# Kernel optimization log

Measured on AMD Instinct MI355X. Metric: run time of the kernel, lower is better.

Reference implementation:

```python
import jax, jax.numpy as jnp
import numpy as np

B, S, HID = 2, 2048, 2048
H, KVH, D = 16, 2, 256
ROT = 64  # head_dim * partial_rotary_factor (0.25)
EPS = 1e-6


def setup_inputs() -> dict:
    key = jax.random.key(0)
    ks = jax.random.split(key, 6)
    hidden_states = jax.random.normal(ks[0], (B, S, HID), dtype=jnp.float32)
    # real partial-RoPE cos/sin, rope_theta = 1e6
    inv_freq = 1.0 / (1e6 ** (np.arange(0, ROT, 2, dtype=np.float32) / ROT))
    pos = np.arange(S, dtype=np.float32)
    freqs = np.outer(pos, inv_freq)                      # [S, ROT/2]
    emb = np.concatenate([freqs, freqs], axis=-1)        # [S, ROT]
    cos = jnp.broadcast_to(jnp.asarray(np.cos(emb)), (B, S, ROT))
    sin = jnp.broadcast_to(jnp.asarray(np.sin(emb)), (B, S, ROT))
    sc = 0.02
    Wq = jax.random.normal(ks[1], (HID, H * D * 2), dtype=jnp.float32) * sc
    Wk = jax.random.normal(ks[2], (HID, KVH * D), dtype=jnp.float32) * sc
    Wv = jax.random.normal(ks[3], (HID, KVH * D), dtype=jnp.float32) * sc
    Wo = jax.random.normal(ks[4], (H * D, HID), dtype=jnp.float32) * sc
    q_norm_w = jnp.zeros((D,), dtype=jnp.float32)
    k_norm_w = jnp.zeros((D,), dtype=jnp.float32)
    return dict(hidden_states=hidden_states, cos=cos, sin=sin, Wq=Wq, Wk=Wk,
                Wv=Wv, Wo=Wo, q_norm_w=q_norm_w, k_norm_w=k_norm_w)


def _rms_norm(x, w):
    x32 = x.astype(jnp.float32)
    out = x32 * jax.lax.rsqrt(jnp.mean(x32 * x32, axis=-1, keepdims=True) + EPS)
    return (out * (1.0 + w.astype(jnp.float32))).astype(x.dtype)


def _rotate_half(x):
    x1, x2 = jnp.split(x, 2, axis=-1)
    return jnp.concatenate([-x2, x1], axis=-1)


def _apply_rope(x, cos, sin):
    # x: [B,S,N,D]; cos/sin: [B,S,ROT] -> unsqueeze head dim
    c = cos[:, :, None, :]
    s = sin[:, :, None, :]
    x_rot, x_pass = x[..., :ROT], x[..., ROT:]
    x_rot = x_rot * c + _rotate_half(x_rot) * s
    return jnp.concatenate([x_rot, x_pass], axis=-1)


def reference(hidden_states, cos, sin, Wq, Wk, Wv, Wo, q_norm_w, k_norm_w):
    b, s, _ = hidden_states.shape
    # gated Q projection: view as (b,s,H,2D), chunk last dim into query + gate
    qg = (hidden_states @ Wq).reshape(b, s, H, 2 * D)
    q, gate = qg[..., :D], qg[..., D:]
    gate = gate.reshape(b, s, H * D)
    k = (hidden_states @ Wk).reshape(b, s, KVH, D)
    v = (hidden_states @ Wv).reshape(b, s, KVH, D)
    # per-head RMSNorm then partial RoPE
    q = _apply_rope(_rms_norm(q, q_norm_w), cos, sin)
    k = _apply_rope(_rms_norm(k, k_norm_w), cos, sin)
    # GQA: repeat kv heads
    rep = H // KVH
    k = jnp.repeat(k, rep, axis=2)  # [b,s,H,D]
    v = jnp.repeat(v, rep, axis=2)
    # causal SDPA (bsnd layout)
    scale = 1.0 / jnp.sqrt(jnp.asarray(D, dtype=q.dtype))
    scores = jnp.einsum('bqhd,bkhd->bhqk', q, k) * scale
    causal = jnp.tril(jnp.ones((s, s), dtype=bool))
    scores = jnp.where(causal[None, None], scores, jnp.finfo(scores.dtype).min)
    probs = jax.nn.softmax(scores, axis=-1)
    attn = jnp.einsum('bhqk,bkhd->bqhd', probs, v).reshape(b, s, H * D)
    # output gating + projection
    attn = attn * jax.nn.sigmoid(gate)
    return attn @ Wo
```

## Files before the change

kernel.cpp:

```cpp
#include <hip/hip_runtime.h>
#include <cstdint>
#include <cstddef>

#define S_   2048
#define H_   16
#define KVH_ 2
#define D_   256

typedef __attribute__((ext_vector_type(4))) float          float4v;
typedef __attribute__((ext_vector_type(4))) float          floatx4;
typedef __attribute__((ext_vector_type(8))) unsigned short ushort8v;
typedef __attribute__((ext_vector_type(4))) unsigned short ushort4v;
typedef __attribute__((ext_vector_type(8))) short          short8;

__device__ __forceinline__ float bf2f(unsigned short u){
  union{float f; unsigned int i;} v; v.i = ((unsigned int)u)<<16; return v.f;
}
__device__ __forceinline__ unsigned short f2bf(float f){
  union{float f; unsigned int i;} v; v.f = f;
  unsigned int r = v.i + 0x7FFFu + ((v.i>>16)&1u);
  return (unsigned short)(r>>16);
}
__device__ __forceinline__ void gld16(const void* g, void* l){
  __builtin_amdgcn_global_load_lds(
      (const __attribute__((address_space(1))) unsigned int*)g,
      (__attribute__((address_space(3))) unsigned int*)l, 16, 0, 0);
}

__global__ __launch_bounds__(256) void conv_k(
    const float* __restrict__ in, unsigned short* __restrict__ out)
{
  const size_t i = ((size_t)blockIdx.x*256 + threadIdx.x)*8;
  float4v a0 = *(const float4v*)(in + i), a1 = *(const float4v*)(in + i + 4);
  ushort8v u;
#pragma unroll
  for (int e=0;e<4;e++){ u[e]=f2bf(a0[e]); u[e+4]=f2bf(a1[e]); }
  *(ushort8v*)(out + i) = u;
}

__global__ __launch_bounds__(256) void tconv_k(
    const float* __restrict__ in, unsigned short* __restrict__ out, int K, int N)
{
  __shared__ unsigned short T[64][72];
  const int n0 = blockIdx.x<<6, k0 = blockIdx.y<<6;
  const int t = threadIdx.x, r = t>>2, c = (t&3)<<4;
  const float* ip = in + (size_t)(k0+r)*N + n0 + c;
  float4v a0=*(const float4v*)ip,     a1=*(const float4v*)(ip+4);
  float4v a2=*(const float4v*)(ip+8), a3=*(const float4v*)(ip+12);
  ushort8v u0,u1;
#pragma unroll
  for (int e=0;e<4;e++){ u0[e]=f2bf(a0[e]); u0[e+4]=f2bf(a1[e]);
                         u1[e]=f2bf(a2[e]); u1[e+4]=f2bf(a3[e]); }
  *(ushort8v*)&T[r][c] = u0; *(ushort8v*)&T[r][c+8] = u1;
  __syncthreads();
  ushort8v o0,o1;
#pragma unroll
  for (int j=0;j<8;j++){ o0[j]=T[c+j][r]; o1[j]=T[c+8+j][r]; }
  unsigned short* op = out + (size_t)(n0+r)*K + k0 + c;
  *(ushort8v*)op = o0; *(ushort8v*)(op+8) = o1;
}

template<int MODE>
__global__ __launch_bounds__(256,2) void gemm_k(
    const unsigned short* __restrict__ A, const unsigned short* __restrict__ Bt,
    void* __restrict__ out0, void* __restrict__ out1, int K, int N)
{
  __shared__ unsigned short Ash[2][128*32];
  __shared__ unsigned short Bsh[2][128*32];
  const int tid  = threadIdx.x;
  const int gm   = blockIdx.x<<7, gn = blockIdx.y<<7;
  const int lane = tid & 63, wave = tid >> 6;
  const int quad = lane >> 4, col = lane & 15;
  const int wm   = (wave>>1)<<6, wn = (wave&1)<<6;
  const int rowoff = lane>>2;
  const int chunk  = (lane&3) ^ (rowoff&3);
  const int ra0 = wave<<4, ra1 = 64 + (wave<<4);
  const unsigned short* Ab = A  + (size_t)gm*K;
  const unsigned short* Bb = Bt + (size_t)gn*K;
  const int cf = (quad ^ (col&3))<<3;

  floatx4 acc[4][4];
#pragma unroll
  for (int i=0;i<4;i++)
#pragma unroll
    for (int j=0;j<4;j++) acc[i][j] = (floatx4)0.f;

  const int niter = K>>5;
  {
    const int ko = chunk*8;
    gld16(Ab + (size_t)(ra0+rowoff)*K + ko, &Ash[0][ra0*32]);
    gld16(Ab + (size_t)(ra1+rowoff)*K + ko, &Ash[0][ra1*32]);
    gld16(Bb + (size_t)(ra0+rowoff)*K + ko, &Bsh[0][ra0*32]);
    gld16(Bb + (size_t)(ra1+rowoff)*K + ko, &Bsh[0][ra1*32]);
  }
  for (int it=0; it<niter; ++it){
    const int buf = it&1;
    __syncthreads();
    if (it+1 < niter){
      const int ko = (it+1)*32 + chunk*8;
      gld16(Ab + (size_t)(ra0+rowoff)*K + ko, &Ash[buf^1][ra0*32]);
      gld16(Ab + (size_t)(ra1+rowoff)*K + ko, &Ash[buf^1][ra1*32]);
      gld16(Bb + (size_t)(ra0+rowoff)*K + ko, &Bsh[buf^1][ra0*32]);
      gld16(Bb + (size_t)(ra1+rowoff)*K + ko, &Bsh[buf^1][ra1*32]);
    }
    short8 af[4], bfr[4];
#pragma unroll
    for (int mi=0;mi<4;mi++) af[mi]  = *(const short8*)&Ash[buf][(wm+mi*16+col)*32 + cf];
#pragma unroll
    for (int ni=0;ni<4;ni++) bfr[ni] = *(const short8*)&Bsh[buf][(wn+ni*16+col)*32 + cf];
#pragma unroll
    for (int mi=0;mi<4;mi++)
#pragma unroll
      for (int ni=0;ni<4;ni++)
        acc[mi][ni] = __builtin_amdgcn_mfma_f32_16x16x32_bf16(af[mi], bfr[ni], acc[mi][ni], 0,0,0);
  }

#pragma unroll
  for (int mi=0;mi<4;mi++){
#pragma unroll
    for (int r=0;r<4;r++){
      const int m = gm + wm + mi*16 + quad*4 + r;
      const int b = m >> 11, s = m & 2047;
#pragma unroll
      for (int ni=0;ni<4;ni++){
        const int n = gn + wn + ni*16 + col;
        const float v = acc[mi][ni][r];
        if (MODE==0){
          if (n < 8192){
            const int h = n >> 9, dd = n & 511;
            if (dd < 256)
              ((unsigned short*)out0)[(((size_t)b*H_ + h)*S_ + s)*D_ + dd] = f2bf(v);
            else
              ((unsigned short*)out1)[((size_t)m*H_ + h)*D_ + (dd-256)] = f2bf(v);
          } else {
            const int n2 = n - 8192;
            if (n2 < 512){
              const int kvh = n2 >> 8, dd = n2 & 255;
              ((unsigned short*)out0)[(size_t)(67108864/2) + (((size_t)b*KVH_ + kvh)*S_ + s)*D_ + dd] = f2bf(v);
            } else {
              const int nv2 = n2 - 512;
              const int kvh = nv2 >> 8, dd = nv2 & 255;
              ((unsigned short*)out0)[(size_t)(71303168/2) + ((((size_t)b*KVH_ + kvh)*64 + (s>>5))*256 + dd)*32 + (s&31)] = f2bf(v);
            }
          }
        } else {
          ((float*)out0)[(size_t)m*N + n] = v;
        }
      }
    }
  }
}

__global__ __launch_bounds__(256,2) void normrope_k(
    unsigned short* __restrict__ x, const float* __restrict__ w,
    const float* __restrict__ cosp, const float* __restrict__ sinp, int heads)
{
  const int lane = threadIdx.x & 63;
  const int row  = blockIdx.x*4 + (threadIdx.x>>6);
  const int s    = row & (S_-1);
  const int b    = (row / S_) / heads;
  unsigned short* xp = x + (size_t)row * D_;
  const int d = lane*4;
  ushort4v xv = *(const ushort4v*)(xp + d);
  float v0=bf2f(xv[0]), v1=bf2f(xv[1]), v2=bf2f(xv[2]), v3=bf2f(xv[3]);
  float ss = v0*v0+v1*v1+v2*v2+v3*v3;
#pragma unroll
  for (int off=1; off<64; off<<=1) ss += __shfl_xor(ss, off, 64);
  const float rstd = rsqrtf(ss*(1.f/256.f) + 1e-6f);
  float nv[4] = { v0*rstd*(1.f+w[d]),   v1*rstd*(1.f+w[d+1]),
                  v2*rstd*(1.f+w[d+2]), v3*rstd*(1.f+w[d+3]) };
  float ov[4];
#pragma unroll
  for (int j=0;j<4;j++){
    const float other = __shfl_xor(nv[j], 8, 64);
    float o = nv[j];
    if (lane < 16){
      const float c  = cosp[((size_t)b*S_+s)*64 + d + j];
      const float sn = sinp[((size_t)b*S_+s)*64 + d + j];
      o = (lane < 8) ? (nv[j]*c - other*sn) : (nv[j]*c + other*sn);
    }
    ov[j] = o;
  }
  ushort4v ou;
#pragma unroll
  for (int j=0;j<4;j++) ou[j] = f2bf(ov[j]);
  *(ushort4v*)(xp + d) = ou;
}

__global__ __launch_bounds__(256,2) void flash_k(
    const unsigned short* __restrict__ qb, const unsigned short* __restrict__ kbp,
    const unsigned short* __restrict__ vtp, const unsigned short* __restrict__ gb,
    unsigned short* __restrict__ ob)
{
  __shared__ unsigned short SH[2*8192 + 2*8192 + 4*2*640];
  unsigned short* Kb0 = SH;
  unsigned short* Vb0 = SH + 16384;
  const int gid = blockIdx.x;
  const int p   = gid & 7;
  const int h   = (gid>>3) & 15;
  const int b   = gid >> 7;
  const int kvh = h >> 3;
  const int tid = threadIdx.x, wave = tid>>6, lane = tid&63;
  const int quad = lane>>4, col = lane&15;
  unsigned short* Psh = SH + 32768 + wave*1280;

  int kOff[4], vOff[4];
#pragma unroll
  for (int j=0;j<4;j++){
    const int krow = wave*8 + j*2 + (lane>>5);
    kOff[j] = krow*256 + ((lane&31) ^ (krow&7))*8;
    const int vrow = wave*64 + j*16 + (lane>>2);
    vOff[j] = vrow*32 + ((lane&3) ^ (vrow&3))*8;
  }
  const unsigned short* Kg = kbp + ((size_t)b*KVH_ + kvh)*S_*D_;
  const unsigned short* Vg = vtp + ((size_t)b*KVH_ + kvh)*S_*D_;

  for (int sp=0; sp<2; ++sp){
    const int qt = sp ? (15-p) : p;
    const int qw = qt*128 + wave*32;
    const int nch = 4*qt + 4;

    short8 qf[2][8];
#pragma unroll
    for (int m=0;m<2;m++){
      const unsigned short* qr = qb + (((size_t)b*H_ + h)*S_ + (qw + m*16 + col))*D_;
#pragma unroll
      for (int dc=0; dc<8; ++dc) qf[m][dc] = *(const short8*)(qr + dc*32 + quad*8);
    }
    floatx4 O[2][16];
#pragma unroll
    for (int m=0;m<2;m++)
#pragma unroll
      for (int i=0;i<16;i++) O[m][i] = (floatx4)0.f;
    float lacc[2][4] = {{0.f,0.f,0.f,0.f},{0.f,0.f,0.f,0.f}};

    __syncthreads();
#pragma unroll
    for (int j=0;j<4;j++){
      gld16(Kg + kOff[j], Kb0 + wave*2048 + j*512);
      gld16(Vg + vOff[j], Vb0 + wave*2048 + j*512);
    }

    int buf = 0;
    for (int kc=0; kc<nch; ++kc){
      __syncthreads();
      if (kc+1 < nch){
        const unsigned short* kg = Kg + (size_t)(kc+1)*8192;
        const unsigned short* vg = Vg + (size_t)(kc+1)*8192;
        unsigned short* kl = Kb0 + (buf^1)*8192 + wave*2048;
        unsigned short* vl = Vb0 + (buf^1)*8192 + wave*2048;
#pragma unroll
        for (int j=0;j<4;j++){
          gld16(kg + kOff[j], kl + j*512);
          gld16(vg + vOff[j], vl + j*512);
        }
      }
      const unsigned short* Ksh = Kb0 + buf*8192;
      const unsigned short* Vt  = Vb0 + buf*8192;

      floatx4 sc[2][2];
#pragma unroll
      for (int m=0;m<2;m++){ sc[m][0]=(floatx4)0.f; sc[m][1]=(floatx4)0.f; }
#pragma unroll
      for (int dc=0; dc<8; ++dc){
#pragma unroll
        for (int nt=0;nt<2;nt++){
          const int row = nt*16+col;
          short8 kf = *(const short8*)&Ksh[row*256 + (((dc*4+quad) ^ (row&7))<<3)];
          sc[0][nt] = __builtin_amdgcn_mfma_f32_16x16x32_bf16(qf[0][dc], kf, sc[0][nt], 0,0,0);
          sc[1][nt] = __builtin_amdgcn_mfma_f32_16x16x32_bf16(qf[1][dc], kf, sc[1][nt], 0,0,0);
        }
      }
      short8 pf[2];
#pragma unroll
      for (int m=0;m<2;m++){
#pragma unroll
        for (int r=0;r<4;r++){
          const int q = qw + m*16 + quad*4 + r;
          float psum = 0.f;
#pragma unroll
          for (int nt=0;nt<2;nt++){
            const int kv = kc*32 + nt*16 + col;
            const float pv = (kv<=q) ? __expf(sc[m][nt][r]*0.0625f) : 0.f;
            psum += pv;
            Psh[m*640 + (quad*4+r)*40 + nt*16 + col] = f2bf(pv);
          }
          lacc[m][r] += psum;
        }
        pf[m] = *(const short8*)&Psh[m*640 + col*40 + quad*8];
      }
#pragma unroll
      for (int nc=0;nc<16;nc++){
        const int row = nc*16+col;
        short8 vf = *(const short8*)&Vt[row*32 + ((quad ^ (row&3))<<3)];
        O[0][nc] = __builtin_amdgcn_mfma_f32_16x16x32_bf16(pf[0], vf, O[0][nc], 0,0,0);
        O[1][nc] = __builtin_amdgcn_mfma_f32_16x16x32_bf16(pf[1], vf, O[1][nc], 0,0,0);
      }
      buf ^= 1;
    }

    __syncthreads();
    unsigned short* rep = SH + wave*8192;
#pragma unroll
    for (int m=0;m<2;m++){
#pragma unroll
      for (int r=0;r<4;r++){
        float s = lacc[m][r];
        s += __shfl_xor(s,1,64); s += __shfl_xor(s,2,64);
        s += __shfl_xor(s,4,64); s += __shfl_xor(s,8,64);
        const float inv = 1.f/s;
        const int rrow = (m*16 + quad*4 + r)*256;
#pragma unroll
        for (int nc=0;nc<16;nc++)
          rep[rrow + nc*16 + col] = f2bf(O[m][nc][r]*inv);
      }
    }
#pragma unroll
    for (int j=0;j<16;j++){
      const int e  = j*512 + lane*8;
      const int ql = j*2 + (lane>>5);
      const int d  = (lane&31)*8;
      ushort8v ov = *(const ushort8v*)&rep[e];
      const size_t base = (((size_t)b*S_ + (qt*128 + wave*32 + ql))*H_ + h)*D_ + d;
      ushort8v gv = *(const ushort8v*)(gb + base);
      ushort8v wv;
#pragma unroll
      for (int k=0;k<8;k++){
        const float gvf = bf2f(gv[k]);
        const float sg  = 1.f/(1.f + __expf(-gvf));
        wv[k] = f2bf(bf2f(ov[k])*sg);
      }
      *(ushort8v*)(ob + base) = wv;
    }
  }
}

extern "C" void kernel_launch(void* const* d_in, const int* in_sizes, int n_in,
                              void* d_out, int out_size, void* d_ws, size_t ws_size,
                              hipStream_t stream)
{
  const float* hs   = (const float*)d_in[0];
  const float* cosp = (const float*)d_in[1];
  const float* sinp = (const float*)d_in[2];
  const float* Wq   = (const float*)d_in[3];
  const float* Wk   = (const float*)d_in[4];
  const float* Wv   = (const float*)d_in[5];
  const float* Wo   = (const float*)d_in[6];
  const float* qw   = (const float*)d_in[7];
  const float* kw   = (const float*)d_in[8];
  float* out = (float*)d_out;

  char* w = (char*)d_ws;
  unsigned short* q_bf  = (unsigned short*)(w);
  unsigned short* gate  = (unsigned short*)(w + 33554432);
  unsigned short* k_bf  = (unsigned short*)(w + 67108864);
  unsigned short* v_t   = (unsigned short*)(w + 71303168);
  unsigned short* hs_bf = (unsigned short*)(w + 75497472);
  unsigned short* wq_t  = (unsigned short*)(w + 92274688);
  unsigned short* wkv_t = (unsigned short*)(w + 125829120);
  unsigned short* wo_t  = (unsigned short*)(w + 92274688);
  unsigned short* attn  = gate;

  conv_k<<<4096, 256, 0, stream>>>(hs, hs_bf);
  tconv_k<<<dim3(128,32), 256, 0, stream>>>(Wq, wq_t, 2048, 8192);
  tconv_k<<<dim3(8,32),   256, 0, stream>>>(Wk, wkv_t, 2048, 512);
  tconv_k<<<dim3(8,32),   256, 0, stream>>>(Wv, wkv_t + (size_t)512*2048, 2048, 512);
  gemm_k<0><<<dim3(32,72), 256, 0, stream>>>(hs_bf, wq_t, q_bf, gate, 2048, 9216);
  tconv_k<<<dim3(32,64), 256, 0, stream>>>(Wo, wo_t, 4096, 2048);
  normrope_k<<<(2*H_*S_)/4,   256, 0, stream>>>(q_bf, qw, cosp, sinp, H_);
  normrope_k<<<(2*KVH_*S_)/4, 256, 0, stream>>>(k_bf, kw, cosp, sinp, KVH_);
  flash_k<<<dim3(256), 256, 0, stream>>>(q_bf, k_bf, v_t, gate, attn);
  gemm_k<3><<<dim3(32,16), 256, 0, stream>>>(attn, wo_t, out, nullptr, 4096, 2048);
}
```

Baseline: 709.6 us.

## Halve flash query tile to double block count; remap GEMM block indices

The flash-attention kernel now has each wave handle 16 query rows instead of 32. Query tiles shrink to 64 rows, so the grid grows from 256 to 512 blocks, which gives better occupancy and load balance across the CUs, and register pressure from the O accumulators is halved. The trade-off is that each block reuses its loaded K/V tiles across fewer query rows, so K/V traffic doubles. The GEMM kernels switch to a 1D grid with a swizzled block-to-tile mapping that groups M tiles, aiming for better L2 reuse of the B operand.

```diff
diff --git a/kernel.cpp b/kernel.cpp
--- a/kernel.cpp
+++ b/kernel.cpp
@@ -67,8 +67,10 @@
 {
   __shared__ unsigned short Ash[2][128*32];
   __shared__ unsigned short Bsh[2][128*32];
+  const int bid  = blockIdx.x;
+  const int gm   = ((bid&7)*4 + ((bid>>3)&3))<<7;
+  const int gn   = (bid>>5)<<7;
   const int tid  = threadIdx.x;
-  const int gm   = blockIdx.x<<7, gn = blockIdx.y<<7;
   const int lane = tid & 63, wave = tid >> 6;
   const int quad = lane >> 4, col = lane & 15;
   const int wm   = (wave>>1)<<6, wn = (wave&1)<<6;
@@ -192,17 +194,17 @@
     const unsigned short* __restrict__ vtp, const unsigned short* __restrict__ gb,
     unsigned short* __restrict__ ob)
 {
-  __shared__ unsigned short SH[2*8192 + 2*8192 + 4*2*640];
+  __shared__ unsigned short SH[2*8192 + 2*8192 + 4*640];
   unsigned short* Kb0 = SH;
   unsigned short* Vb0 = SH + 16384;
   const int gid = blockIdx.x;
-  const int p   = gid & 7;
-  const int h   = (gid>>3) & 15;
-  const int b   = gid >> 7;
+  const int p   = gid & 15;
+  const int h   = (gid>>4) & 15;
+  const int b   = gid >> 8;
   const int kvh = h >> 3;
   const int tid = threadIdx.x, wave = tid>>6, lane = tid&63;
   const int quad = lane>>4, col = lane&15;
-  unsigned short* Psh = SH + 32768 + wave*1280;
+  unsigned short* Psh = SH + 32768 + wave*640;
 
   int kOff[4], vOff[4];
 #pragma unroll
@@ -216,23 +218,20 @@
   const unsigned short* Vg = vtp + ((size_t)b*KVH_ + kvh)*S_*D_;
 
   for (int sp=0; sp<2; ++sp){
-    const int qt = sp ? (15-p) : p;
-    const int qw = qt*128 + wave*32;
-    const int nch = 4*qt + 4;
-
-    short8 qf[2][8];
-#pragma unroll
-    for (int m=0;m<2;m++){
-      const unsigned short* qr = qb + (((size_t)b*H_ + h)*S_ + (qw + m*16 + col))*D_;
-#pragma unroll
-      for (int dc=0; dc<8; ++dc) qf[m][dc] = *(const short8*)(qr + dc*32 + quad*8);
-    }
-    floatx4 O[2][16];
-#pragma unroll
-    for (int m=0;m<2;m++)
-#pragma unroll
-      for (int i=0;i<16;i++) O[m][i] = (floatx4)0.f;
-    float lacc[2][4] = {{0.f,0.f,0.f,0.f},{0.f,0.f,0.f,0.f}};
+    const int qt = sp ? (31-p) : p;
+    const int q0 = qt*64 + wave*16;
+    const int nch = 2*qt + 2;
+
+    short8 qf[8];
+    {
+      const unsigned short* qr = qb + (((size_t)b*H_ + h)*S_ + (q0+col))*D_;
+#pragma unroll
+      for (int dc=0; dc<8; ++dc) qf[dc] = *(const short8*)(qr + dc*32 + quad*8);
+    }
+    floatx4 O[16];
+#pragma unroll
+    for (int i=0;i<16;i++) O[i] = (floatx4)0.f;
+    float lacc[4] = {0.f,0.f,0.f,0.f};
 
     __syncthreads();
 #pragma unroll
@@ -258,70 +257,60 @@
       const unsigned short* Ksh = Kb0 + buf*8192;
       const unsigned short* Vt  = Vb0 + buf*8192;
 
-      floatx4 sc[2][2];
-#pragma unroll
-      for (int m=0;m<2;m++){ sc[m][0]=(floatx4)0.f; sc[m][1]=(floatx4)0.f; }
+      floatx4 sc[2];
+      sc[0]=(floatx4)0.f; sc[1]=(floatx4)0.f;
 #pragma unroll
       for (int dc=0; dc<8; ++dc){
 #pragma unroll
         for (int nt=0;nt<2;nt++){
           const int row = nt*16+col;
           short8 kf = *(const short8*)&Ksh[row*256 + (((dc*4+quad) ^ (row&7))<<3)];
-          sc[0][nt] = __builtin_amdgcn_mfma_f32_16x16x32_bf16(qf[0][dc], kf, sc[0][nt], 0,0,0);
-          sc[1][nt] = __builtin_amdgcn_mfma_f32_16x16x32_bf16(qf[1][dc], kf, sc[1][nt], 0,0,0);
+          sc[nt] = __builtin_amdgcn_mfma_f32_16x16x32_bf16(qf[dc], kf, sc[nt], 0,0,0);
         }
       }
-      short8 pf[2];
-#pragma unroll
-      for (int m=0;m<2;m++){
-#pragma unroll
-        for (int r=0;r<4;r++){
-          const int q = qw + m*16 + quad*4 + r;
-          float psum = 0.f;
-#pragma unroll
-          for (int nt=0;nt<2;nt++){
-            const int kv = kc*32 + nt*16 + col;
-            const float pv = (kv<=q) ? __expf(sc[m][nt][r]*0.0625f) : 0.f;
-            psum += pv;
-            Psh[m*640 + (quad*4+r)*40 + nt*16 + col] = f2bf(pv);
-          }
-          lacc[m][r] += psum;
+#pragma unroll
+      for (int r=0;r<4;r++){
+        const int q = q0 + quad*4 + r;
+        float psum = 0.f;
+#pragma unroll
+        for (int nt=0;nt<2;nt++){
+          const int kv = kc*32 + nt*16 + col;
+          const float pv = (kv<=q) ? __expf(sc[nt][r]*0.0625f) : 0.f;
+          psum += pv;
+          Psh[(quad*4+r)*40 + nt*16 + col] = f2bf(pv);
         }
-        pf[m] = *(const short8*)&Psh[m*640 + col*40 + quad*8];
-      }
+        lacc[r] += psum;
+      }
+      short8 pf = *(const short8*)&Psh[col*40 + quad*8];
 #pragma unroll
       for (int nc=0;nc<16;nc++){
         const int row = nc*16+col;
         short8 vf = *(const short8*)&Vt[row*32 + ((quad ^ (row&3))<<3)];
-        O[0][nc] = __builtin_amdgcn_mfma_f32_16x16x32_bf16(pf[0], vf, O[0][nc], 0,0,0);
-        O[1][nc] = __builtin_amdgcn_mfma_f32_16x16x32_bf16(pf[1], vf, O[1][nc], 0,0,0);
+        O[nc] = __builtin_amdgcn_mfma_f32_16x16x32_bf16(pf, vf, O[nc], 0,0,0);
       }
       buf ^= 1;
     }
 
     __syncthreads();
-    unsigned short* rep = SH + wave*8192;
-#pragma unroll
-    for (int m=0;m<2;m++){
-#pragma unroll
-      for (int r=0;r<4;r++){
-        float s = lacc[m][r];
-        s += __shfl_xor(s,1,64); s += __shfl_xor(s,2,64);
-        s += __shfl_xor(s,4,64); s += __shfl_xor(s,8,64);
-        const float inv = 1.f/s;
-        const int rrow = (m*16 + quad*4 + r)*256;
-#pragma unroll
-        for (int nc=0;nc<16;nc++)
-          rep[rrow + nc*16 + col] = f2bf(O[m][nc][r]*inv);
-      }
-    }
-#pragma unroll
-    for (int j=0;j<16;j++){
+    unsigned short* rep = SH + wave*4096;
+#pragma unroll
+    for (int r=0;r<4;r++){
+      float s = lacc[r];
+      s += __shfl_xor(s,1,64); s += __shfl_xor(s,2,64);
+      s += __shfl_xor(s,4,64); s += __shfl_xor(s,8,64);
+      const float inv = 1.f/s;
+      const int rrow = (quad*4 + r)*256;
+#pragma unroll
+      for (int nc=0;nc<16;nc++)
+        rep[rrow + nc*16 + col] = f2bf(O[nc][r]*inv);
+    }
+#pragma unroll
+    for (int j=0;j<8;j++){
       const int e  = j*512 + lane*8;
       const int ql = j*2 + (lane>>5);
       const int d  = (lane&31)*8;
       ushort8v ov = *(const ushort8v*)&rep[e];
-      const size_t base = (((size_t)b*S_ + (qt*128 + wave*32 + ql))*H_ + h)*D_ + d;
+      const size_t base = (((size_t)b*S_ + (q0 + ql))*H_ + h)*D_ + d;
       ushort8v gv = *(const ushort8v*)(gb + base);
       ushort8v wv;
 #pragma unroll
@@ -365,10 +354,10 @@
   tconv_k<<<dim3(128,32), 256, 0, stream>>>(Wq, wq_t, 2048, 8192);
   tconv_k<<<dim3(8,32),   256, 0, stream>>>(Wk, wkv_t, 2048, 512);
   tconv_k<<<dim3(8,32),   256, 0, stream>>>(Wv, wkv_t + (size_t)512*2048, 2048, 512);
-  gemm_k<0><<<dim3(32,72), 256, 0, stream>>>(hs_bf, wq_t, q_bf, gate, 2048, 9216);
+  gemm_k<0><<<dim3(2304), 256, 0, stream>>>(hs_bf, wq_t, q_bf, gate, 2048, 9216);
   tconv_k<<<dim3(32,64), 256, 0, stream>>>(Wo, wo_t, 4096, 2048);
   normrope_k<<<(2*H_*S_)/4,   256, 0, stream>>>(q_bf, qw, cosp, sinp, H_);
   normrope_k<<<(2*KVH_*S_)/4, 256, 0, stream>>>(k_bf, kw, cosp, sinp, KVH_);
-  flash_k<<<dim3(256), 256, 0, stream>>>(q_bf, k_bf, v_t, gate, attn);
-  gemm_k<3><<<dim3(32,16), 256, 0, stream>>>(attn, wo_t, out, nullptr, 4096, 2048);
-}
+  flash_k<<<dim3(512), 256, 0, stream>>>(q_bf, k_bf, v_t, gate, attn);
+  gemm_k<3><<<dim3(512), 256, 0, stream>>>(attn, wo_t, out, nullptr, 4096, 2048);
+}
```

After: 604.7 us. 1.17x faster.
